# Performance work log

Hardware: AMD Instinct MI355X
Metric: run time of the kernel (lower is better)

Reference implementation:

```python
import jax, jax.numpy as jnp
import numpy as np

B, N, DIM, HEADS = 1024, 144, 192, 6
W0, W1, W2 = 2, 6, 12
L = (2 * W2 - 1) * W1 * W1 * W0 * W0  # 3312 unique relative positions


def setup_inputs() -> dict:
    key = jax.random.key(0)
    ks = jax.random.split(key, 8)
    x = jax.random.normal(ks[0], (B, N, DIM), jnp.float32)
    w1 = jax.random.normal(ks[1], (DIM, 3 * DIM), jnp.float32) * 0.02
    b1 = jnp.zeros((3 * DIM,), jnp.float32)
    w2 = jax.random.normal(ks[2], (DIM, DIM), jnp.float32) * 0.02
    b2 = jnp.zeros((DIM,), jnp.float32)
    bias_table = jax.random.normal(ks[3], (L, HEADS), jnp.float32) * 0.02
    position_index = jax.random.randint(ks[4], (N, N), 0, L, jnp.int32)
    mask = jax.random.randint(ks[5], (N, N), 0, 2, jnp.int32)
    return {"x": x, "w1": w1, "b1": b1, "w2": w2, "b2": b2,
            "bias_table": bias_table, "position_index": position_index,
            "mask": mask}


def reference(x, w1, b1, w2, b2, bias_table, position_index, mask):
    Bq, Nq, D = x.shape
    H = HEADS
    d = D // H
    scale = d ** -0.5
    # qkv projection: [B,N,3D] -> [B,N,3,H,d]
    qkv = (x @ w1 + b1).reshape(Bq, Nq, 3, H, d)
    q = qkv[:, :, 0].transpose(0, 2, 1, 3)  # [B,H,N,d]
    k = qkv[:, :, 1].transpose(0, 2, 1, 3)
    v = qkv[:, :, 2].transpose(0, 2, 1, 3)
    attn = jnp.einsum('bhnd,bhmd->bhnm', q * scale, k)  # [B,H,N,N]
    # earth-specific relative bias gathered per (query, key) position pair
    bias = bias_table[position_index].transpose(2, 0, 1)  # [H,N,N]
    attn = attn + bias
    attn = jnp.where(mask == 0, jnp.float32(-1e9), attn)
    attn = jax.nn.softmax(attn, axis=-1)
    out = jnp.einsum('bhnm,bhmd->bhnd', attn, v)  # [B,H,N,d]
    out = out.transpose(0, 2, 1, 3).reshape(Bq, Nq, D)  # merge heads
    return out @ w2 + b2
```

## Files before the change

### kernel.cpp

```cpp
#include <hip/hip_runtime.h>

#define BATCH 1024
#define SEQ   144
#define DIM   192
#define NH    6
#define HD    32
#define SCALE 0.17677669529663687f

typedef __bf16 bf16x8 __attribute__((ext_vector_type(8)));
typedef __bf16 bf16x4 __attribute__((ext_vector_type(4)));
typedef float  f32x4  __attribute__((ext_vector_type(4)));

__device__ __forceinline__ void lds_barrier() {
    __builtin_amdgcn_sched_barrier(0);
    asm volatile("s_waitcnt lgkmcnt(0)" ::: "memory");
    __builtin_amdgcn_s_barrier();
    __builtin_amdgcn_sched_barrier(0);
}

#define WS_W1T   0
#define WS_W2T   221184
#define WS_B1S   294912
#define WS_BM    297216
#define WS_QF    546048
#define WS_KF    57169152
#define WS_VT    113792256

#define BH_STRIDE 4608

__global__ __launch_bounds__(256) void k_prep(
        const float* __restrict__ w1, const float* __restrict__ w2,
        const float* __restrict__ b1, const float* __restrict__ bt,
        const int* __restrict__ pidx, const int* __restrict__ mask,
        char* __restrict__ ws) {
    __bf16* w1t = (__bf16*)(ws + WS_W1T);
    __bf16* w2t = (__bf16*)(ws + WS_W2T);
    float*  b1s = (float*)(ws + WS_B1S);
    __bf16* bm  = (__bf16*)(ws + WS_BM);
    const int blk = blockIdx.x, t = threadIdx.x;
    if (blk < 432) {
        int idx = blk * 256 + t;
        int k = idx / 576, c = idx % 576;
        float v = w1[idx] * (c < 192 ? SCALE : 1.0f);
        w1t[c * 192 + k] = (__bf16)v;
    } else if (blk < 576) {
        int idx = (blk - 432) * 256 + t;
        int k = idx / 192, n = idx % 192;
        w2t[n * 192 + k] = (__bf16)w2[idx];
    } else if (blk < 657) {
        int idx = (blk - 576) * 256 + t;
        int p = pidx[idx];
        float add = (mask[idx] == 0) ? -1e9f : 0.0f;
#pragma unroll
        for (int h = 0; h < NH; ++h)
            bm[h * 20736 + idx] = (__bf16)(bt[p * NH + h] + add);
    } else {
        for (int c = t; c < 576; c += 256)
            b1s[c] = b1[c] * (c < 192 ? SCALE : 1.0f);
    }
}

__global__ __launch_bounds__(256, 3) void k_qkv(
        const float* __restrict__ x, char* __restrict__ ws) {
    const __bf16* w1t = (const __bf16*)(ws + WS_W1T);
    const float*  b1s = (const float*)(ws + WS_B1S);
    __bf16* qf  = (__bf16*)(ws + WS_QF);
    __bf16* kf  = (__bf16*)(ws + WS_KF);
    __bf16* vtf = (__bf16*)(ws + WS_VT);

    __shared__ __bf16 As[2][16 * 200];
    __shared__ __bf16 Stg[4][16 * 56];

    const int tid = threadIdx.x;
    const int w = tid >> 6, lane = tid & 63, lr = tid & 15, lg = (tid & 63) >> 4;

    const int phys = blockIdx.x;
    const int logical = (phys & 7) * 384 + (phys >> 3);
    const int b  = logical / 3;
    const int cg = logical % 3;
    const f32x4 zf = {0.f, 0.f, 0.f, 0.f};

    bf16x8 bW[3][6];
    float bcol[3];
#pragma unroll
    for (int i = 0; i < 3; ++i) {
        int col = cg * 192 + (w * 3 + i) * 16 + lr;
        bcol[i] = b1s[col];
#pragma unroll
        for (int kk = 0; kk < 6; ++kk)
            bW[i][kk] = *(const bf16x8*)(w1t + (col * 192 + kk * 32 + lg * 8));
    }

    __bf16* qk_dst = (cg == 0) ? qf : kf;
    __bf16* stg = Stg[w];

    const int c0 = tid;
    auto stage = [&](int t, int buf) {
        const float* src = x + ((size_t)b * SEQ + t * 16) * DIM;
#pragma unroll
        for (int j = 0; j < 3; ++j) {
            int c = c0 + j * 256;
            int row = c / 48, c4 = (c % 48) * 4;
            f32x4 v = *(const f32x4*)&src[row * DIM + c4];
            bf16x4 pk;
            pk[0] = (__bf16)v[0]; pk[1] = (__bf16)v[1];
            pk[2] = (__bf16)v[2]; pk[3] = (__bf16)v[3];
            *(bf16x4*)&As[buf][row * 200 + c4] = pk;
        }
    };

    stage(0, 0);

    for (int t = 0; t < 9; ++t) {
        f32x4 nxt[3];
        if (t < 8) {
            const float* src = x + ((size_t)b * SEQ + (t + 1) * 16) * DIM;
#pragma unroll
            for (int j = 0; j < 3; ++j) {
                int c = c0 + j * 256;
                int row = c / 48, c4 = (c % 48) * 4;
                nxt[j] = *(const f32x4*)&src[row * DIM + c4];
            }
        }
        lds_barrier();
        const __bf16* A = As[t & 1];
        f32x4 acc[3];
#pragma unroll
        for (int i = 0; i < 3; ++i) acc[i] = zf;
#pragma unroll
        for (int kk = 0; kk < 6; ++kk) {
            bf16x8 aF = *(const bf16x8*)&A[lr * 200 + kk * 32 + lg * 8];
#pragma unroll
            for (int i = 0; i < 3; ++i)
                acc[i] = __builtin_amdgcn_mfma_f32_16x16x32_bf16(aF, bW[i][kk], acc[i], 0, 0, 0);
        }

        if (cg < 2) {
#pragma unroll
            for (int i = 0; i < 3; ++i)
#pragma unroll
                for (int r = 0; r < 4; ++r)
                    stg[(lg * 4 + r) * 56 + i * 16 + lr] = (__bf16)(acc[i][r] + bcol[i]);
#pragma unroll
            for (int rep = 0; rep < 2; ++rep) {
                int c = lane + rep * 64;
                if (rep == 0 || lane < 32) {
                    int m = c / 6, c8 = c % 6;
                    bf16x8 v = *(bf16x8*)&stg[m * 56 + c8 * 8];
                    int j2 = w * 48 + c8 * 8;
                    int h = j2 >> 5, j = j2 & 31;
                    size_t bh = (size_t)b * NH + h;
                    *(bf16x8*)&qk_dst[bh * BH_STRIDE + (size_t)(t * 16 + m) * HD + j] = v;
                }
            }
        } else {
            const int m = t * 16 + lg * 4;
#pragma unroll
            for (int i = 0; i < 3; ++i) {
                int j2 = (w * 3 + i) * 16 + lr;
                int h = j2 >> 5, j = j2 & 31;
                size_t bh = (size_t)b * NH + h;
                bf16x4 pk;
#pragma unroll
                for (int r = 0; r < 4; ++r) pk[r] = (__bf16)(acc[i][r] + bcol[i]);
                *(bf16x4*)&vtf[bh * BH_STRIDE + (size_t)j * SEQ + m] = pk;
            }
        }

        if (t < 8) {
#pragma unroll
            for (int j = 0; j < 3; ++j) {
                int c = c0 + j * 256;
                int row = c / 48, c4 = (c % 48) * 4;
                f32x4 v = nxt[j];
                bf16x4 pk;
                pk[0] = (__bf16)v[0]; pk[1] = (__bf16)v[1];
                pk[2] = (__bf16)v[2]; pk[3] = (__bf16)v[3];
                *(bf16x4*)&As[(t + 1) & 1][row * 200 + c4] = pk;
            }
        }
    }
}

__global__ __launch_bounds__(576, 2) void k_attn3(char* __restrict__ ws) {
    const __bf16* bmB = (const __bf16*)(ws + WS_BM);
    const __bf16* qf  = (const __bf16*)(ws + WS_QF);
    const __bf16* kf  = (const __bf16*)(ws + WS_KF);
    const __bf16* vtf = (const __bf16*)(ws + WS_VT);
    __bf16* opre = (__bf16*)(ws + WS_QF);

    __shared__ char smem[32768];
    __bf16* Ks  = (__bf16*)smem;
    __bf16* Vt  = (__bf16*)(smem + 11520);
    __bf16* Pws = (__bf16*)(smem + 21248);

    const int bx = blockIdx.x;
    const int h  = bx >> 10;
    const int b  = bx & 1023;
    const size_t bh = (size_t)(b * NH + h);

    const int tid  = threadIdx.x;
    const int w    = tid >> 6;
    const int lane = tid & 63;
    const int lr   = lane & 15;
    const int lg   = lane >> 4;
    const int m0   = w * 16;
    const f32x4 zf = {0.f, 0.f, 0.f, 0.f};
    const bf16x8 zb = {(__bf16)0.f,(__bf16)0.f,(__bf16)0.f,(__bf16)0.f,
                       (__bf16)0.f,(__bf16)0.f,(__bf16)0.f,(__bf16)0.f};

    bf16x8 kch = *(const bf16x8*)(kf  + bh * BH_STRIDE + (size_t)tid * 8);
    bf16x8 vch = *(const bf16x8*)(vtf + bh * BH_STRIDE + (size_t)tid * 8);
    bf16x8 qF  = *(const bf16x8*)(qf  + bh * BH_STRIDE + (size_t)(m0 + lr) * HD + lg * 8);
    bf16x4 bb[9];
    {
        const __bf16* bmh = bmB + h * 20736 + (m0 + lr) * SEQ;
#pragma unroll
        for (int i = 0; i < 9; ++i) bb[i] = *(const bf16x4*)&bmh[i * 16 + lg * 4];
    }

    *(bf16x8*)&Ks[(tid >> 2) * 40 + (tid & 3) * 8] = kch;
    {
        int vr = tid / 18, vc = tid % 18;
        *(bf16x8*)&Vt[vr * 152 + vc * 8] = vch;
    }
    lds_barrier();

    f32x4 st[9];
#pragma unroll
    for (int i = 0; i < 9; ++i) {
        bf16x8 aF = *(bf16x8*)&Ks[(i * 16 + lr) * 40 + lg * 8];
        st[i] = __builtin_amdgcn_mfma_f32_16x16x32_bf16(aF, qF, zf, 0, 0, 0);
    }
    float mx = -3.0e38f;
#pragma unroll
    for (int i = 0; i < 9; ++i)
#pragma unroll
        for (int r = 0; r < 4; ++r) {
            st[i][r] += (float)bb[i][r];
            mx = fmaxf(mx, st[i][r]);
        }
    mx = fmaxf(mx, __shfl_xor(mx, 16));
    mx = fmaxf(mx, __shfl_xor(mx, 32));
    float sum = 0.f;
#pragma unroll
    for (int i = 0; i < 9; ++i)
#pragma unroll
        for (int r = 0; r < 4; ++r) {
            float e = __expf(st[i][r] - mx);
            st[i][r] = e;
            sum += e;
        }
    sum += __shfl_xor(sum, 16);
    sum += __shfl_xor(sum, 32);
    float inv = 1.f / sum;
#pragma unroll
    for (int i = 0; i < 9; ++i)
#pragma unroll
        for (int r = 0; r < 4; ++r) st[i][r] *= inv;

    __bf16* Pw = Pws + w * 640;
    f32x4 o0 = zf, o1 = zf;
#pragma unroll
    for (int s = 0; s < 4; ++s) {
#pragma unroll
        for (int d = 0; d < 2; ++d) {
            int ii = 2 * s + d;
            bf16x4 pk;
#pragma unroll
            for (int r = 0; r < 4; ++r) pk[r] = (__bf16)st[ii][r];
            *(bf16x4*)&Pw[lr * 40 + d * 16 + lg * 4] = pk;
        }
        bf16x8 aP  = *(bf16x8*)&Pw[lr * 40 + lg * 8];
        bf16x8 v0F = *(bf16x8*)&Vt[lr * 152 + s * 32 + lg * 8];
        bf16x8 v1F = *(bf16x8*)&Vt[(16 + lr) * 152 + s * 32 + lg * 8];
        o0 = __builtin_amdgcn_mfma_f32_16x16x32_bf16(aP, v0F, o0, 0, 0, 0);
        o1 = __builtin_amdgcn_mfma_f32_16x16x32_bf16(aP, v1F, o1, 0, 0, 0);
    }
    {
        bf16x4 pk;
#pragma unroll
        for (int r = 0; r < 4; ++r) pk[r] = (__bf16)st[8][r];
        *(bf16x4*)&Pw[lr * 40 + lg * 4] = pk;
        bf16x8 aP = zb, v0F = zb, v1F = zb;
        if (lg < 2) {
            aP  = *(bf16x8*)&Pw[lr * 40 + lg * 8];
            v0F = *(bf16x8*)&Vt[lr * 152 + 128 + lg * 8];
            v1F = *(bf16x8*)&Vt[(16 + lr) * 152 + 128 + lg * 8];
        }
        o0 = __builtin_amdgcn_mfma_f32_16x16x32_bf16(aP, v0F, o0, 0, 0, 0);
        o1 = __builtin_amdgcn_mfma_f32_16x16x32_bf16(aP, v1F, o1, 0, 0, 0);
    }

#pragma unroll
    for (int r = 0; r < 4; ++r) {
        Pw[(lg * 4 + r) * 40 + lr]      = (__bf16)o0[r];
        Pw[(lg * 4 + r) * 40 + 16 + lr] = (__bf16)o1[r];
    }
    {
        int row = lane >> 2, c = lane & 3;
        bf16x8 ov = *(bf16x8*)&Pw[row * 40 + c * 8];
        *(bf16x8*)&opre[bh * BH_STRIDE + (size_t)(m0 + row) * HD + c * 8] = ov;
    }
}

__global__ __launch_bounds__(256, 3) void k_proj(
        const char* __restrict__ ws, const float* __restrict__ b2,
        float* __restrict__ out) {
    const __bf16* opre = (const __bf16*)(ws + WS_QF);
    const __bf16* w2t  = (const __bf16*)(ws + WS_W2T);
    __shared__ __bf16 As[2][16 * 200];

    const int tid = threadIdx.x;
    const int w = tid >> 6, lr = tid & 15, lg = (tid & 63) >> 4;
    const int b = blockIdx.x;
    const f32x4 zf = {0.f, 0.f, 0.f, 0.f};

    bf16x8 bW[3][6];
    float bcol[3];
#pragma unroll
    for (int i = 0; i < 3; ++i) {
        int col = (w * 3 + i) * 16 + lr;
        bcol[i] = b2[col];
#pragma unroll
        for (int kk = 0; kk < 6; ++kk)
            bW[i][kk] = *(const bf16x8*)(w2t + (col * 192 + kk * 32 + lg * 8));
    }

    auto src_of = [&](int t, int c) -> const __bf16* {
        int lrow = c / 24, c8 = c % 24;
        int h = c8 >> 2, col32 = (c8 & 3) * 8;
        return opre + ((size_t)(b * NH + h)) * BH_STRIDE
                    + (size_t)(t * 16 + lrow) * HD + col32;
    };
    auto dst_of = [&](int buf, int c) -> __bf16* {
        int lrow = c / 24, c8 = c % 24;
        return &As[buf][lrow * 200 + c8 * 8];
    };

    {
        *(bf16x8*)dst_of(0, tid) = *(const bf16x8*)src_of(0, tid);
        if (tid < 128)
            *(bf16x8*)dst_of(0, tid + 256) = *(const bf16x8*)src_of(0, tid + 256);
    }

    for (int t = 0; t < 9; ++t) {
        bf16x8 n0, n1;
        if (t < 8) {
            n0 = *(const bf16x8*)src_of(t + 1, tid);
            if (tid < 128) n1 = *(const bf16x8*)src_of(t + 1, tid + 256);
        }
        lds_barrier();
        const __bf16* A = As[t & 1];
        f32x4 acc[3];
#pragma unroll
        for (int i = 0; i < 3; ++i) acc[i] = zf;
#pragma unroll
        for (int kk = 0; kk < 6; ++kk) {
            bf16x8 aF = *(const bf16x8*)&A[lr * 200 + kk * 32 + lg * 8];
#pragma unroll
            for (int i = 0; i < 3; ++i)
                acc[i] = __builtin_amdgcn_mfma_f32_16x16x32_bf16(aF, bW[i][kk], acc[i], 0, 0, 0);
        }
        size_t row0 = (size_t)b * SEQ + t * 16;
#pragma unroll
        for (int i = 0; i < 3; ++i) {
            int col = (w * 3 + i) * 16 + lr;
#pragma unroll
            for (int r = 0; r < 4; ++r)
                out[(row0 + lg * 4 + r) * DIM + col] = acc[i][r] + bcol[i];
        }
        if (t < 8) {
            *(bf16x8*)dst_of((t + 1) & 1, tid) = n0;
            if (tid < 128) *(bf16x8*)dst_of((t + 1) & 1, tid + 256) = n1;
        }
    }
}

extern "C" void kernel_launch(void* const* d_in, const int* in_sizes, int n_in,
                              void* d_out, int out_size, void* d_ws, size_t ws_size,
                              hipStream_t stream) {
    const float* x    = (const float*)d_in[0];
    const float* w1   = (const float*)d_in[1];
    const float* b1   = (const float*)d_in[2];
    const float* w2   = (const float*)d_in[3];
    const float* b2   = (const float*)d_in[4];
    const float* bt   = (const float*)d_in[5];
    const int*   pidx = (const int*)d_in[6];
    const int*   mask = (const int*)d_in[7];
    float* out = (float*)d_out;
    char*  ws  = (char*)d_ws;

    k_prep<<<658, 256, 0, stream>>>(w1, w2, b1, bt, pidx, mask, ws);
    k_qkv<<<3072, 256, 0, stream>>>(x, ws);
    k_attn3<<<BATCH * NH, 576, 0, stream>>>(ws);
    k_proj<<<BATCH, 256, 0, stream>>>(ws, b2, out);
}
```

Before: 191.1 us.

## Merge QKV column-group blocks into one block per batch sharing staged x

The QKV projection now launches one 768-thread block per batch element, with 12 waves covering the Q, K and V column groups, instead of three 256-thread blocks. The staged bf16 x tile in shared memory is shared by all three groups, removing the redundant global reads and conversions of x. Each thread stages one vector per tile instead of three. This trades away the L2-friendly block remapping and raises register-pressure risk through an aggressive launch-bounds occupancy hint.

```diff
diff --git a/kernel.cpp b/kernel.cpp
--- a/kernel.cpp
+++ b/kernel.cpp
@@ -60,7 +60,7 @@
     }
 }
 
-__global__ __launch_bounds__(256, 3) void k_qkv(
+__global__ __launch_bounds__(768, 6) void k_qkv(
         const float* __restrict__ x, char* __restrict__ ws) {
     const __bf16* w1t = (const __bf16*)(ws + WS_W1T);
     const float*  b1s = (const float*)(ws + WS_B1S);
@@ -69,22 +69,23 @@
     __bf16* vtf = (__bf16*)(ws + WS_VT);
 
     __shared__ __bf16 As[2][16 * 200];
-    __shared__ __bf16 Stg[4][16 * 56];
-
-    const int tid = threadIdx.x;
-    const int w = tid >> 6, lane = tid & 63, lr = tid & 15, lg = (tid & 63) >> 4;
-
-    const int phys = blockIdx.x;
-    const int logical = (phys & 7) * 384 + (phys >> 3);
-    const int b  = logical / 3;
-    const int cg = logical % 3;
+    __shared__ __bf16 Stg[8][16 * 56];
+
+    const int tid  = threadIdx.x;
+    const int w    = tid >> 6;
+    const int lane = tid & 63;
+    const int lr   = lane & 15;
+    const int lg   = lane >> 4;
+    const int cg   = w >> 2;
+    const int wp   = w & 3;
+    const int b    = blockIdx.x;
     const f32x4 zf = {0.f, 0.f, 0.f, 0.f};
 
     bf16x8 bW[3][6];
     float bcol[3];
 #pragma unroll
     for (int i = 0; i < 3; ++i) {
-        int col = cg * 192 + (w * 3 + i) * 16 + lr;
+        int col = cg * 192 + (wp * 3 + i) * 16 + lr;
         bcol[i] = b1s[col];
 #pragma unroll
         for (int kk = 0; kk < 6; ++kk)
@@ -92,35 +93,26 @@
     }
 
     __bf16* qk_dst = (cg == 0) ? qf : kf;
-    __bf16* stg = Stg[w];
-
-    const int c0 = tid;
+    __bf16* stg = (cg < 2) ? Stg[w] : nullptr;
+
     auto stage = [&](int t, int buf) {
         const float* src = x + ((size_t)b * SEQ + t * 16) * DIM;
-#pragma unroll
-        for (int j = 0; j < 3; ++j) {
-            int c = c0 + j * 256;
-            int row = c / 48, c4 = (c % 48) * 4;
-            f32x4 v = *(const f32x4*)&src[row * DIM + c4];
-            bf16x4 pk;
-            pk[0] = (__bf16)v[0]; pk[1] = (__bf16)v[1];
-            pk[2] = (__bf16)v[2]; pk[3] = (__bf16)v[3];
-            *(bf16x4*)&As[buf][row * 200 + c4] = pk;
-        }
+        int row = tid / 48, c4 = (tid % 48) * 4;
+        f32x4 v = *(const f32x4*)&src[row * DIM + c4];
+        bf16x4 pk;
+        pk[0] = (__bf16)v[0]; pk[1] = (__bf16)v[1];
+        pk[2] = (__bf16)v[2]; pk[3] = (__bf16)v[3];
+        *(bf16x4*)&As[buf][row * 200 + c4] = pk;
     };
 
     stage(0, 0);
 
     for (int t = 0; t < 9; ++t) {
-        f32x4 nxt[3];
+        f32x4 nxt;
         if (t < 8) {
             const float* src = x + ((size_t)b * SEQ + (t + 1) * 16) * DIM;
-#pragma unroll
-            for (int j = 0; j < 3; ++j) {
-                int c = c0 + j * 256;
-                int row = c / 48, c4 = (c % 48) * 4;
-                nxt[j] = *(const f32x4*)&src[row * DIM + c4];
-            }
+            int row = tid / 48, c4 = (tid % 48) * 4;
+            nxt = *(const f32x4*)&src[row * DIM + c4];
         }
         lds_barrier();
         const __bf16* A = As[t & 1];
@@ -147,7 +139,7 @@
                 if (rep == 0 || lane < 32) {
                     int m = c / 6, c8 = c % 6;
                     bf16x8 v = *(bf16x8*)&stg[m * 56 + c8 * 8];
-                    int j2 = w * 48 + c8 * 8;
+                    int j2 = wp * 48 + c8 * 8;
                     int h = j2 >> 5, j = j2 & 31;
                     size_t bh = (size_t)b * NH + h;
                     *(bf16x8*)&qk_dst[bh * BH_STRIDE + (size_t)(t * 16 + m) * HD + j] = v;
@@ -157,7 +149,7 @@
             const int m = t * 16 + lg * 4;
 #pragma unroll
             for (int i = 0; i < 3; ++i) {
-                int j2 = (w * 3 + i) * 16 + lr;
+                int j2 = (wp * 3 + i) * 16 + lr;
                 int h = j2 >> 5, j = j2 & 31;
                 size_t bh = (size_t)b * NH + h;
                 bf16x4 pk;
@@ -168,16 +160,12 @@
         }
 
         if (t < 8) {
-#pragma unroll
-            for (int j = 0; j < 3; ++j) {
-                int c = c0 + j * 256;
-                int row = c / 48, c4 = (c % 48) * 4;
-                f32x4 v = nxt[j];
-                bf16x4 pk;
-                pk[0] = (__bf16)v[0]; pk[1] = (__bf16)v[1];
-                pk[2] = (__bf16)v[2]; pk[3] = (__bf16)v[3];
-                *(bf16x4*)&As[(t + 1) & 1][row * 200 + c4] = pk;
-            }
+            int row = tid / 48, c4 = (tid % 48) * 4;
+            f32x4 v = nxt;
+            bf16x4 pk;
+            pk[0] = (__bf16)v[0]; pk[1] = (__bf16)v[1];
+            pk[2] = (__bf16)v[2]; pk[3] = (__bf16)v[3];
+            *(bf16x4*)&As[(t + 1) & 1][row * 200 + c4] = pk;
         }
     }
 }
@@ -392,7 +380,7 @@
     char*  ws  = (char*)d_ws;
 
     k_prep<<<658, 256, 0, stream>>>(w1, w2, b1, bt, pidx, mask, ws);
-    k_qkv<<<3072, 256, 0, stream>>>(x, ws);
+    k_qkv<<<BATCH, 768, 0, stream>>>(x, ws);
     k_attn3<<<BATCH * NH, 576, 0, stream>>>(ws);
     k_proj<<<BATCH, 256, 0, stream>>>(ws, b2, out);
 }
```

Result: slower. 390.7 us (+104.4%).

## Fuse attention and output projection into one per-batch kernel looping over heads

Applied to the files above, without the earlier changes.

Merges the attention kernel and the output projection kernel into a single kernel with one block per batch element that loops over the six heads. Each head's attention output stays in LDS and is immediately multiplied by the matching slice of the projection weights, accumulating into twelve register tiles. This removes the bf16 round trip of the pre-projection activations through global memory and one kernel launch. In exchange, per-block parallelism drops sixfold (1024 blocks instead of 6144), the head loop is serialized with extra barriers, W2 is re-read from global or cache for each head, and register pressure rises under a tighter launch bound.

```diff
diff --git a/kernel.cpp b/kernel.cpp
--- a/kernel.cpp
+++ b/kernel.cpp
@@ -182,22 +182,21 @@
     }
 }
 
-__global__ __launch_bounds__(576, 2) void k_attn3(char* __restrict__ ws) {
+__global__ __launch_bounds__(576, 3) void k_attnproj(
+        const char* __restrict__ ws, const float* __restrict__ b2,
+        float* __restrict__ out) {
     const __bf16* bmB = (const __bf16*)(ws + WS_BM);
     const __bf16* qf  = (const __bf16*)(ws + WS_QF);
     const __bf16* kf  = (const __bf16*)(ws + WS_KF);
     const __bf16* vtf = (const __bf16*)(ws + WS_VT);
-    __bf16* opre = (__bf16*)(ws + WS_QF);
+    const __bf16* w2t = (const __bf16*)(ws + WS_W2T);
 
     __shared__ char smem[32768];
     __bf16* Ks  = (__bf16*)smem;
     __bf16* Vt  = (__bf16*)(smem + 11520);
     __bf16* Pws = (__bf16*)(smem + 21248);
 
-    const int bx = blockIdx.x;
-    const int h  = bx >> 10;
-    const int b  = bx & 1023;
-    const size_t bh = (size_t)(b * NH + h);
+    const int b = blockIdx.x;
 
     const int tid  = threadIdx.x;
     const int w    = tid >> 6;
@@ -209,171 +208,131 @@
     const bf16x8 zb = {(__bf16)0.f,(__bf16)0.f,(__bf16)0.f,(__bf16)0.f,
                        (__bf16)0.f,(__bf16)0.f,(__bf16)0.f,(__bf16)0.f};
 
-    bf16x8 kch = *(const bf16x8*)(kf  + bh * BH_STRIDE + (size_t)tid * 8);
-    bf16x8 vch = *(const bf16x8*)(vtf + bh * BH_STRIDE + (size_t)tid * 8);
-    bf16x8 qF  = *(const bf16x8*)(qf  + bh * BH_STRIDE + (size_t)(m0 + lr) * HD + lg * 8);
-    bf16x4 bb[9];
-    {
-        const __bf16* bmh = bmB + h * 20736 + (m0 + lr) * SEQ;
-#pragma unroll
-        for (int i = 0; i < 9; ++i) bb[i] = *(const bf16x4*)&bmh[i * 16 + lg * 4];
-    }
-
-    *(bf16x8*)&Ks[(tid >> 2) * 40 + (tid & 3) * 8] = kch;
-    {
-        int vr = tid / 18, vc = tid % 18;
-        *(bf16x8*)&Vt[vr * 152 + vc * 8] = vch;
-    }
-    lds_barrier();
-
-    f32x4 st[9];
-#pragma unroll
-    for (int i = 0; i < 9; ++i) {
-        bf16x8 aF = *(bf16x8*)&Ks[(i * 16 + lr) * 40 + lg * 8];
-        st[i] = __builtin_amdgcn_mfma_f32_16x16x32_bf16(aF, qF, zf, 0, 0, 0);
-    }
-    float mx = -3.0e38f;
-#pragma unroll
-    for (int i = 0; i < 9; ++i)
+    __bf16* Pw = Pws + w * 640;
+    f32x4 outacc[12];
+#pragma unroll
+    for (int n = 0; n < 12; ++n) outacc[n] = zf;
+
+#pragma unroll 1
+    for (int h = 0; h < NH; ++h) {
+        const size_t bh = (size_t)b * NH + h;
+
+        bf16x8 kch = *(const bf16x8*)(kf  + bh * BH_STRIDE + (size_t)tid * 8);
+        bf16x8 vch = *(const bf16x8*)(vtf + bh * BH_STRIDE + (size_t)tid * 8);
+        bf16x8 qF  = *(const bf16x8*)(qf  + bh * BH_STRIDE + (size_t)(m0 + lr) * HD + lg * 8);
+        bf16x4 bb[9];
+        {
+            const __bf16* bmh = bmB + h * 20736 + (m0 + lr) * SEQ;
+#pragma unroll
+            for (int i = 0; i < 9; ++i) bb[i] = *(const bf16x4*)&bmh[i * 16 + lg * 4];
+        }
+
+        lds_barrier();
+
+        *(bf16x8*)&Ks[(tid >> 2) * 40 + (tid & 3) * 8] = kch;
+        {
+            int vr = tid / 18, vc = tid % 18;
+            *(bf16x8*)&Vt[vr * 152 + vc * 8] = vch;
+        }
+        lds_barrier();
+
+        f32x4 st[9];
+#pragma unroll
+        for (int i = 0; i < 9; ++i) {
+            bf16x8 aF = *(bf16x8*)&Ks[(i * 16 + lr) * 40 + lg * 8];
+            st[i] = __builtin_amdgcn_mfma_f32_16x16x32_bf16(aF, qF, zf, 0, 0, 0);
+        }
+        float mx = -3.0e38f;
+#pragma unroll
+        for (int i = 0; i < 9; ++i)
+#pragma unroll
+            for (int r = 0; r < 4; ++r) {
+                st[i][r] += (float)bb[i][r];
+                mx = fmaxf(mx, st[i][r]);
+            }
+        mx = fmaxf(mx, __shfl_xor(mx, 16));
+        mx = fmaxf(mx, __shfl_xor(mx, 32));
+        float sum = 0.f;
+#pragma unroll
+        for (int i = 0; i < 9; ++i)
+#pragma unroll
+            for (int r = 0; r < 4; ++r) {
+                float e = __expf(st[i][r] - mx);
+                st[i][r] = e;
+                sum += e;
+            }
+        sum += __shfl_xor(sum, 16);
+        sum += __shfl_xor(sum, 32);
+        float inv = 1.f / sum;
+#pragma unroll
+        for (int i = 0; i < 9; ++i)
+#pragma unroll
+            for (int r = 0; r < 4; ++r) st[i][r] *= inv;
+
+        f32x4 o0 = zf, o1 = zf;
+#pragma unroll
+        for (int s = 0; s < 4; ++s) {
+#pragma unroll
+            for (int d = 0; d < 2; ++d) {
+                int ii = 2 * s + d;
+                bf16x4 pk;
+#pragma unroll
+                for (int r = 0; r < 4; ++r) pk[r] = (__bf16)st[ii][r];
+                *(bf16x4*)&Pw[lr * 40 + d * 16 + lg * 4] = pk;
+            }
+            bf16x8 aP  = *(bf16x8*)&Pw[lr * 40 + lg * 8];
+            bf16x8 v0F = *(bf16x8*)&Vt[lr * 152 + s * 32 + lg * 8];
+            bf16x8 v1F = *(bf16x8*)&Vt[(16 + lr) * 152 + s * 32 + lg * 8];
+            o0 = __builtin_amdgcn_mfma_f32_16x16x32_bf16(aP, v0F, o0, 0, 0, 0);
+            o1 = __builtin_amdgcn_mfma_f32_16x16x32_bf16(aP, v1F, o1, 0, 0, 0);
+        }
+        {
+            bf16x4 pk;
+#pragma unroll
+            for (int r = 0; r < 4; ++r) pk[r] = (__bf16)st[8][r];
+            *(bf16x4*)&Pw[lr * 40 + lg * 4] = pk;
+            bf16x8 aP = zb, v0F = zb, v1F = zb;
+            if (lg < 2) {
+                aP  = *(bf16x8*)&Pw[lr * 40 + lg * 8];
+                v0F = *(bf16x8*)&Vt[lr * 152 + 128 + lg * 8];
+                v1F = *(bf16x8*)&Vt[(16 + lr) * 152 + 128 + lg * 8];
+            }
+            o0 = __builtin_amdgcn_mfma_f32_16x16x32_bf16(aP, v0F, o0, 0, 0, 0);
+            o1 = __builtin_amdgcn_mfma_f32_16x16x32_bf16(aP, v1F, o1, 0, 0, 0);
+        }
+
 #pragma unroll
         for (int r = 0; r < 4; ++r) {
-            st[i][r] += (float)bb[i][r];
-            mx = fmaxf(mx, st[i][r]);
-        }
-    mx = fmaxf(mx, __shfl_xor(mx, 16));
-    mx = fmaxf(mx, __shfl_xor(mx, 32));
-    float sum = 0.f;
-#pragma unroll
-    for (int i = 0; i < 9; ++i)
-#pragma unroll
-        for (int r = 0; r < 4; ++r) {
-            float e = __expf(st[i][r] - mx);
-            st[i][r] = e;
-            sum += e;
-        }
-    sum += __shfl_xor(sum, 16);
-    sum += __shfl_xor(sum, 32);
-    float inv = 1.f / sum;
-#pragma unroll
-    for (int i = 0; i < 9; ++i)
-#pragma unroll
-        for (int r = 0; r < 4; ++r) st[i][r] *= inv;
-
-    __bf16* Pw = Pws + w * 640;
-    f32x4 o0 = zf, o1 = zf;
-#pragma unroll
-    for (int s = 0; s < 4; ++s) {
-#pragma unroll
-        for (int d = 0; d < 2; ++d) {
-            int ii = 2 * s + d;
-            bf16x4 pk;
-#pragma unroll
-            for (int r = 0; r < 4; ++r) pk[r] = (__bf16)st[ii][r];
-            *(bf16x4*)&Pw[lr * 40 + d * 16 + lg * 4] = pk;
-        }
-        bf16x8 aP  = *(bf16x8*)&Pw[lr * 40 + lg * 8];
-        bf16x8 v0F = *(bf16x8*)&Vt[lr * 152 + s * 32 + lg * 8];
-        bf16x8 v1F = *(bf16x8*)&Vt[(16 + lr) * 152 + s * 32 + lg * 8];
-        o0 = __builtin_amdgcn_mfma_f32_16x16x32_bf16(aP, v0F, o0, 0, 0, 0);
-        o1 = __builtin_amdgcn_mfma_f32_16x16x32_bf16(aP, v1F, o1, 0, 0, 0);
-    }
-    {
-        bf16x4 pk;
-#pragma unroll
-        for (int r = 0; r < 4; ++r) pk[r] = (__bf16)st[8][r];
-        *(bf16x4*)&Pw[lr * 40 + lg * 4] = pk;
-        bf16x8 aP = zb, v0F = zb, v1F = zb;
-        if (lg < 2) {
-            aP  = *(bf16x8*)&Pw[lr * 40 + lg * 8];
-            v0F = *(bf16x8*)&Vt[lr * 152 + 128 + lg * 8];
-            v1F = *(bf16x8*)&Vt[(16 + lr) * 152 + 128 + lg * 8];
-        }
-        o0 = __builtin_amdgcn_mfma_f32_16x16x32_bf16(aP, v0F, o0, 0, 0, 0);
-        o1 = __builtin_amdgcn_mfma_f32_16x16x32_bf16(aP, v1F, o1, 0, 0, 0);
-    }
-
-#pragma unroll
-    for (int r = 0; r < 4; ++r) {
-        Pw[(lg * 4 + r) * 40 + lr]      = (__bf16)o0[r];
-        Pw[(lg * 4 + r) * 40 + 16 + lr] = (__bf16)o1[r];
-    }
-    {
-        int row = lane >> 2, c = lane & 3;
-        bf16x8 ov = *(bf16x8*)&Pw[row * 40 + c * 8];
-        *(bf16x8*)&opre[bh * BH_STRIDE + (size_t)(m0 + row) * HD + c * 8] = ov;
-    }
-}
-
-__global__ __launch_bounds__(256, 3) void k_proj(
-        const char* __restrict__ ws, const float* __restrict__ b2,
-        float* __restrict__ out) {
-    const __bf16* opre = (const __bf16*)(ws + WS_QF);
-    const __bf16* w2t  = (const __bf16*)(ws + WS_W2T);
-    __shared__ __bf16 As[2][16 * 200];
-
-    const int tid = threadIdx.x;
-    const int w = tid >> 6, lr = tid & 15, lg = (tid & 63) >> 4;
-    const int b = blockIdx.x;
-    const f32x4 zf = {0.f, 0.f, 0.f, 0.f};
-
-    bf16x8 bW[3][6];
-    float bcol[3];
-#pragma unroll
-    for (int i = 0; i < 3; ++i) {
-        int col = (w * 3 + i) * 16 + lr;
-        bcol[i] = b2[col];
-#pragma unroll
-        for (int kk = 0; kk < 6; ++kk)
-            bW[i][kk] = *(const bf16x8*)(w2t + (col * 192 + kk * 32 + lg * 8));
-    }
-
-    auto src_of = [&](int t, int c) -> const __bf16* {
-        int lrow = c / 24, c8 = c % 24;
-        int h = c8 >> 2, col32 = (c8 & 3) * 8;
-        return opre + ((size_t)(b * NH + h)) * BH_STRIDE
-                    + (size_t)(t * 16 + lrow) * HD + col32;
-    };
-    auto dst_of = [&](int buf, int c) -> __bf16* {
-        int lrow = c / 24, c8 = c % 24;
-        return &As[buf][lrow * 200 + c8 * 8];
-    };
-
-    {
-        *(bf16x8*)dst_of(0, tid) = *(const bf16x8*)src_of(0, tid);
-        if (tid < 128)
-            *(bf16x8*)dst_of(0, tid + 256) = *(const bf16x8*)src_of(0, tid + 256);
-    }
-
-    for (int t = 0; t < 9; ++t) {
-        bf16x8 n0, n1;
-        if (t < 8) {
-            n0 = *(const bf16x8*)src_of(t + 1, tid);
-            if (tid < 128) n1 = *(const bf16x8*)src_of(t + 1, tid + 256);
-        }
-        lds_barrier();
-        const __bf16* A = As[t & 1];
-        f32x4 acc[3];
-#pragma unroll
-        for (int i = 0; i < 3; ++i) acc[i] = zf;
-#pragma unroll
-        for (int kk = 0; kk < 6; ++kk) {
-            bf16x8 aF = *(const bf16x8*)&A[lr * 200 + kk * 32 + lg * 8];
-#pragma unroll
-            for (int i = 0; i < 3; ++i)
-                acc[i] = __builtin_amdgcn_mfma_f32_16x16x32_bf16(aF, bW[i][kk], acc[i], 0, 0, 0);
-        }
-        size_t row0 = (size_t)b * SEQ + t * 16;
-#pragma unroll
-        for (int i = 0; i < 3; ++i) {
-            int col = (w * 3 + i) * 16 + lr;
-#pragma unroll
-            for (int r = 0; r < 4; ++r)
-                out[(row0 + lg * 4 + r) * DIM + col] = acc[i][r] + bcol[i];
-        }
-        if (t < 8) {
-            *(bf16x8*)dst_of((t + 1) & 1, tid) = n0;
-            if (tid < 128) *(bf16x8*)dst_of((t + 1) & 1, tid + 256) = n1;
-        }
+            Pw[(lg * 4 + r) * 40 + lr]      = (__bf16)o0[r];
+            Pw[(lg * 4 + r) * 40 + 16 + lr] = (__bf16)o1[r];
+        }
+
+        {
+            bf16x8 aO = *(bf16x8*)&Pw[lr * 40 + lg * 8];
+#pragma unroll
+            for (int half = 0; half < 2; ++half) {
+                bf16x8 bW2[6];
+#pragma unroll
+                for (int q = 0; q < 6; ++q) {
+                    int n = half * 6 + q;
+                    bW2[q] = *(const bf16x8*)(w2t + ((n * 16 + lr) * 192 + h * 32 + lg * 8));
+                }
+#pragma unroll
+                for (int q = 0; q < 6; ++q) {
+                    int n = half * 6 + q;
+                    outacc[n] = __builtin_amdgcn_mfma_f32_16x16x32_bf16(aO, bW2[q], outacc[n], 0, 0, 0);
+                }
+            }
+        }
+    }
+
+#pragma unroll
+    for (int n = 0; n < 12; ++n) {
+        int col = n * 16 + lr;
+        float bb2 = b2[col];
+#pragma unroll
+        for (int r = 0; r < 4; ++r)
+            out[((size_t)b * SEQ + m0 + lg * 4 + r) * DIM + col] = outacc[n][r] + bb2;
     }
 }
 
@@ -393,6 +352,5 @@
 
     k_prep<<<658, 256, 0, stream>>>(w1, w2, b1, bt, pidx, mask, ws);
     k_qkv<<<3072, 256, 0, stream>>>(x, ws);
-    k_attn3<<<BATCH * NH, 576, 0, stream>>>(ws);
-    k_proj<<<BATCH, 256, 0, stream>>>(ws, b2, out);
-}
+    k_attnproj<<<BATCH, 576, 0, stream>>>(ws, b2, out);
+}
```

Measured after the change: 241.8 us. 1.26x slower.
